# Kernel optimization log

Hardware: AMD Instinct MI355X
Metric: run time of the kernel (lower is better)

Reference implementation:

```python
import jax, jax.numpy as jnp
import numpy as np

N_NODES = 50000
N_EDGES = 800000
D = 128
N_GRAPHS = 128
N_CLASSES = 10
BN_EPS = 1e-5


def setup_inputs() -> dict:
    key = jax.random.key(0)
    ks = jax.random.split(key, 8)
    x = jax.random.normal(ks[0], (N_NODES, D), dtype=jnp.float32)
    edge_index = jax.random.randint(ks[1], (2, N_EDGES), 0, N_NODES, dtype=jnp.int64)
    batch = jnp.sort(jax.random.randint(ks[2], (N_NODES,), 0, N_GRAPHS, dtype=jnp.int64))
    s = 1.0 / np.sqrt(D)
    W1a = jax.random.normal(ks[3], (D, D), dtype=jnp.float32) * s
    W1b = jax.random.normal(ks[4], (D, D), dtype=jnp.float32) * s
    W2a = jax.random.normal(ks[5], (D, D), dtype=jnp.float32) * s
    W2b = jax.random.normal(ks[6], (D, D), dtype=jnp.float32) * s
    Wo = jax.random.normal(ks[7], (D, N_CLASSES), dtype=jnp.float32) * s
    z = jnp.zeros((D,), jnp.float32)
    o = jnp.ones((D,), jnp.float32)
    return dict(x=x, edge_index=edge_index, batch=batch,
                W1a=W1a, b1a=z, W1b=W1b, b1b=z, g1=o, be1=z,
                W2a=W2a, b2a=z, W2b=W2b, b2b=z, g2=o, be2=z,
                Wo=Wo, bo=jnp.zeros((N_CLASSES,), jnp.float32))


def _gin_conv(x, edge_index, Wa, ba, Wb, bb):
    # message passing: gather source features, scatter-add to targets (eps=0)
    msgs = x[edge_index[0]]                                   # [E, D]
    agg = jax.ops.segment_sum(msgs, edge_index[1], num_segments=x.shape[0])
    h = agg + x                                               # (1+eps)*x + sum_j x_j
    h = jnp.maximum(h @ Wa + ba, 0.0)                         # Linear -> ReLU
    return h @ Wb + bb                                        # Linear


def _bn_relu(h, gamma, beta):
    # BatchNorm1d (training mode: batch stats, biased var) + ReLU
    mu = jnp.mean(h, axis=0)
    var = jnp.mean(jnp.square(h - mu), axis=0)
    hn = (h - mu) * jax.lax.rsqrt(var + BN_EPS) * gamma + beta
    return jnp.maximum(hn, 0.0)


def reference(x, edge_index, batch,
              W1a, b1a, W1b, b1b, g1, be1,
              W2a, b2a, W2b, b2b, g2, be2,
              Wo, bo):
    h = _gin_conv(x, edge_index, W1a, b1a, W1b, b1b)
    h = _bn_relu(h, g1, be1)
    h = _gin_conv(h, edge_index, W2a, b2a, W2b, b2b)
    h = _bn_relu(h, g2, be2)
    pooled = jax.ops.segment_sum(h, batch, num_segments=N_GRAPHS)  # global_add_pool
    return pooled @ Wo + bo
```

## Files before the change

kernel.cpp:

```cpp
#include <hip/hip_runtime.h>

typedef __attribute__((ext_vector_type(8))) short bf16x8;
typedef __attribute__((ext_vector_type(4))) float f32x4;
typedef __attribute__((ext_vector_type(2))) float f32x2;
typedef __attribute__((ext_vector_type(2))) unsigned u32x2;
typedef __attribute__((ext_vector_type(4))) unsigned u32x4;

#define N_NODES 50000
#define N_EDGES 800000
#define DIM 128
#define N_GRAPHS 128
#define N_CLASSES 10
#define BN_EPS 1e-5f
#define FBLK ((N_NODES + 63) / 64)
#define FGRID (FBLK / 2)
#define NPART (FBLK * 4)
#define RED_NB 64
#define RED_ROWS ((NPART + RED_NB - 1) / RED_NB)

#define NBUCK 196
#define FILL_NB 400
#define FILL_PER (N_EDGES / FILL_NB)
#define BMAX 6144

#define CVT_NB (N_NODES * 64 / 256)
#define PREPW_NB 256

static __device__ __forceinline__ unsigned short f2bf(float f) {
    unsigned u = __float_as_uint(f);
    u += 0x7FFF + ((u >> 16) & 1);
    return (unsigned short)(u >> 16);
}
static __device__ __forceinline__ float bf_lo(unsigned u) { return __uint_as_float(u << 16); }
static __device__ __forceinline__ float bf_hi(unsigned u) { return __uint_as_float(u & 0xffff0000u); }
static __device__ __forceinline__ unsigned packbf(float a, float b) {
    return (unsigned)f2bf(a) | ((unsigned)f2bf(b) << 16);
}

__global__ __launch_bounds__(256) void prep_all(const f32x2* __restrict__ x,
                                                unsigned* __restrict__ xb,
                                                const float* __restrict__ W0,
                                                const float* __restrict__ W1,
                                                const float* __restrict__ W2,
                                                const float* __restrict__ W3,
                                                unsigned short* __restrict__ wf,
                                                const int* __restrict__ batch,
                                                int* __restrict__ gs,
                                                const int* __restrict__ ei,
                                                int* __restrict__ gbcnt,
                                                int* __restrict__ boff,
                                                int* __restrict__ gcur,
                                                int* __restrict__ ctr_scan) {
    int b = blockIdx.x, tid = threadIdx.x;
    if (b < CVT_NB) {
        int t = b * 256 + tid;
        f32x2 v = x[t];
        xb[t] = packbf(v[0], v[1]);
    } else if (b < CVT_NB + PREPW_NB) {
        int t = (b - CVT_NB) * 256 + tid;
        int m = t >> 14, rem = t & 16383;
        int e = rem & 7, lane = (rem >> 3) & 63, fi = rem >> 9;
        int ks = fi & 3, n = fi >> 2;
        int col = n * 16 + (lane & 15);
        int k = ks * 32 + ((lane >> 4) << 3) + e;
        const float* W = (m == 0) ? W0 : (m == 1) ? W1 : (m == 2) ? W2 : W3;
        wf[t] = f2bf(W[k * DIM + col]);
    } else if (b < CVT_NB + PREPW_NB + FILL_NB) {
        __shared__ int cnt[NBUCK];
        __shared__ int done;
        if (tid < NBUCK) cnt[tid] = 0;
        __syncthreads();
        int e0 = (b - CVT_NB - PREPW_NB) * FILL_PER;
        for (int c = tid; c < FILL_PER; c += 256) {
            int dst = ei[N_EDGES + e0 + c];
            atomicAdd(&cnt[dst >> 8], 1);
        }
        __syncthreads();
        if (tid < NBUCK) atomicAdd(&gbcnt[tid], cnt[tid]);
        __threadfence();
        __syncthreads();
        if (tid == 0) done = atomicAdd(ctr_scan, 1);
        __syncthreads();
        if (done == FILL_NB - 1) {
            __threadfence();
            __shared__ int buf[256];
            int v = (tid < NBUCK) ? gbcnt[tid] : 0;
            buf[tid] = v;
            __syncthreads();
#pragma unroll
            for (int off = 1; off < 256; off <<= 1) {
                int u = (tid >= off) ? buf[tid - off] : 0;
                __syncthreads();
                buf[tid] += u;
                __syncthreads();
            }
            if (tid < NBUCK) { int ex = buf[tid] - v; boff[tid] = ex; gcur[tid] = ex; }
            if (tid == 0) boff[NBUCK] = N_EDGES;
        }
    } else {
        int g = tid;
        if (g > N_GRAPHS) return;
        int lo = 0, hi = N_NODES;
        while (lo < hi) {
            int mid = (lo + hi) >> 1;
            if (batch[mid] < g) lo = mid + 1; else hi = mid;
        }
        gs[g] = lo;
    }
}

__global__ __launch_bounds__(256) void bucket_fill(const int* __restrict__ ei,
                                                   int* __restrict__ gcur,
                                                   unsigned* __restrict__ gbuf) {
    __shared__ unsigned ent[FILL_PER];
    __shared__ unsigned srt[FILL_PER];
    __shared__ int cnt[256], c2[256], lofs[256], gbase[256];
    int tid = threadIdx.x;
    int e0 = blockIdx.x * FILL_PER;
    cnt[tid] = 0; c2[tid] = 0;
    __syncthreads();
    for (int i = tid; i < FILL_PER; i += 256) {
        int src = ei[e0 + i];
        int dst = ei[N_EDGES + e0 + i];
        ent[i] = (unsigned)src | ((unsigned)(dst & 255) << 16) | ((unsigned)(dst >> 8) << 24);
        atomicAdd(&cnt[dst >> 8], 1);
    }
    __syncthreads();
    int v = cnt[tid];
    lofs[tid] = v;
    __syncthreads();
#pragma unroll
    for (int off = 1; off < 256; off <<= 1) {
        int u = (tid >= off) ? lofs[tid - off] : 0;
        __syncthreads();
        lofs[tid] += u;
        __syncthreads();
    }
    int excl = lofs[tid] - v;
    lofs[tid] = excl;
    if (tid < NBUCK && v > 0) gbase[tid] = atomicAdd(&gcur[tid], v);
    __syncthreads();
    for (int i = tid; i < FILL_PER; i += 256) {
        unsigned w = ent[i];
        int b = w >> 24;
        int r = atomicAdd(&c2[b], 1);
        srt[lofs[b] + r] = w;
    }
    __syncthreads();
    for (int i = tid; i < FILL_PER; i += 256) {
        unsigned w = srt[i];
        int b = w >> 24;
        gbuf[gbase[b] + (i - lofs[b])] = w;
    }
}

__global__ __launch_bounds__(256) void csr_build(const unsigned* __restrict__ gbuf,
                                                 const int* __restrict__ boff,
                                                 unsigned short* __restrict__ csr16,
                                                 int* __restrict__ row_start) {
    __shared__ unsigned ent[BMAX];
    __shared__ unsigned short csl[BMAX];
    __shared__ int cnt[256], c2[256], offs[256];
    int b = blockIdx.x, t = threadIdx.x;
    int base = boff[b], n = boff[b + 1] - base;
    for (int i = t; i < n; i += 256) ent[i] = gbuf[base + i];
    cnt[t] = 0; c2[t] = 0;
    __syncthreads();
    for (int i = t; i < n; i += 256) atomicAdd(&cnt[(ent[i] >> 16) & 255], 1);
    __syncthreads();
    int v = cnt[t];
    offs[t] = v;
    __syncthreads();
#pragma unroll
    for (int off = 1; off < 256; off <<= 1) {
        int u = (t >= off) ? offs[t - off] : 0;
        __syncthreads();
        offs[t] += u;
        __syncthreads();
    }
    int excl = offs[t] - v;
    int node = b * 256 + t;
    if (node < N_NODES) row_start[node] = base + excl;
    if (b == NBUCK - 1 && t == 0) row_start[N_NODES] = N_EDGES;
    __syncthreads();
    offs[t] = excl;
    __syncthreads();
    for (int i = t; i < n; i += 256) {
        unsigned w = ent[i];
        int d = (w >> 16) & 255;
        int r = atomicAdd(&c2[d], 1);
        csl[offs[d] + r] = (unsigned short)(w & 0xffffu);
    }
    __syncthreads();
    for (int i = t; i < n; i += 256) csr16[base + i] = csl[i];
}

template <bool BN>
__global__ __launch_bounds__(256) void aggregate_bf(const u32x4* __restrict__ F4,
                                                    u32x4* __restrict__ out,
                                                    const int* __restrict__ row_start,
                                                    const unsigned short* __restrict__ csr16,
                                                    const float* __restrict__ scale,
                                                    const float* __restrict__ shift) {
    int wave = threadIdx.x >> 6, lane = threadIdx.x & 63;
    int v = blockIdx.x * 4 + wave;
    if (v >= N_NODES) return;
    int q = lane >> 4;
    int c8 = lane & 15;
    f32x4 scA, scB, shA, shB;
    if (BN) {
        scA = ((const f32x4*)scale)[c8 * 2];
        scB = ((const f32x4*)scale)[c8 * 2 + 1];
        shA = ((const f32x4*)shift)[c8 * 2];
        shB = ((const f32x4*)shift)[c8 * 2 + 1];
    }
    int e0 = row_start[v];
    int n = row_start[v + 1] - e0;
    int myidx = (lane < n) ? (int)csr16[e0 + lane] : 0;
    int n64 = (n < 64) ? n : 64;

    float a[8] = {0.f, 0.f, 0.f, 0.f, 0.f, 0.f, 0.f, 0.f};
    float bacc[8] = {0.f, 0.f, 0.f, 0.f, 0.f, 0.f, 0.f, 0.f};

#define UNPACK8(U, P)                                                         \
    P[0] = bf_lo(U[0]); P[1] = bf_hi(U[0]); P[2] = bf_lo(U[1]); P[3] = bf_hi(U[1]); \
    P[4] = bf_lo(U[2]); P[5] = bf_hi(U[2]); P[6] = bf_lo(U[3]); P[7] = bf_hi(U[3]);
#define BN8(P)                                                                \
    if (BN) {                                                                 \
        P[0] = fmaxf(P[0] * scA[0] + shA[0], 0.f);                            \
        P[1] = fmaxf(P[1] * scA[1] + shA[1], 0.f);                            \
        P[2] = fmaxf(P[2] * scA[2] + shA[2], 0.f);                            \
        P[3] = fmaxf(P[3] * scA[3] + shA[3], 0.f);                            \
        P[4] = fmaxf(P[4] * scB[0] + shB[0], 0.f);                            \
        P[5] = fmaxf(P[5] * scB[1] + shB[1], 0.f);                            \
        P[6] = fmaxf(P[6] * scB[2] + shB[2], 0.f);                            \
        P[7] = fmaxf(P[7] * scB[3] + shB[3], 0.f);                            \
    }

    if (q == 0) {
        u32x4 u = F4[(size_t)v * 16 + c8];
        float p[8];
        UNPACK8(u, p)
        BN8(p)
#pragma unroll
        for (int k = 0; k < 8; ++k) a[k] += p[k];
    }

    for (int base = 0; base < n64; base += 8) {
        int j0 = base + q, j1 = base + 4 + q;
        int s0 = __shfl(myidx, j0 & 63, 64);
        int s1 = __shfl(myidx, j1 & 63, 64);
        u32x4 ua = F4[(size_t)s0 * 16 + c8];
        u32x4 ub = F4[(size_t)s1 * 16 + c8];
        float p[8], r[8];
        UNPACK8(ua, p)
        UNPACK8(ub, r)
        BN8(p)
        BN8(r)
        if (j0 < n64) {
#pragma unroll
            for (int k = 0; k < 8; ++k) a[k] += p[k];
        }
        if (j1 < n64) {
#pragma unroll
            for (int k = 0; k < 8; ++k) bacc[k] += r[k];
        }
    }
    for (int j = 64 + q; j < n; j += 4) {
        int s = csr16[e0 + j];
        u32x4 ua = F4[(size_t)s * 16 + c8];
        float p[8];
        UNPACK8(ua, p)
        BN8(p)
#pragma unroll
        for (int k = 0; k < 8; ++k) a[k] += p[k];
    }
#pragma unroll
    for (int k = 0; k < 8; ++k) a[k] += bacc[k];
#pragma unroll
    for (int k = 0; k < 8; ++k) {
        a[k] += __shfl_xor(a[k], 16, 64);
        a[k] += __shfl_xor(a[k], 32, 64);
    }
    if (q == 0) {
        u32x4 w;
        w[0] = packbf(a[0], a[1]);
        w[1] = packbf(a[2], a[3]);
        w[2] = packbf(a[4], a[5]);
        w[3] = packbf(a[6], a[7]);
        out[(size_t)v * 16 + c8] = w;
    }
#undef UNPACK8
#undef BN8
}

__global__ __launch_bounds__(256, 3) void fused_layer(
        const unsigned short* __restrict__ A,
        const bf16x8* __restrict__ wfA_g,
        const bf16x8* __restrict__ wfB_g,
        const float* __restrict__ bias_a,
        const float* __restrict__ bias_b,
        unsigned short* __restrict__ out,
        float* __restrict__ psum,
        float* __restrict__ psq, int M) {
    __shared__ bf16x8 wfS[2048];
    __shared__ unsigned short mid[8192];

    int tid = threadIdx.x;
    int w = tid >> 6, lane = tid & 63;
    int cl = lane & 15, kq = lane >> 4;

    bf16x8 wa[8], wb[8];
#pragma unroll
    for (int i = 0; i < 8; ++i) wa[i] = wfA_g[i * 256 + tid];
#pragma unroll
    for (int i = 0; i < 8; ++i) wb[i] = wfB_g[i * 256 + tid];

    for (int t = 0; t < 2; ++t) {
        int tile = blockIdx.x + t * FGRID;
        int rblk = tile * 64;

#pragma unroll
        for (int i = 0; i < 8; ++i) wfS[i * 256 + tid] = wa[i];

        int arow = rblk + w * 16 + cl;
        if (arow >= M) arow = M - 1;
        bf16x8 af[4];
        const unsigned short* Ap = A + (size_t)arow * DIM + kq * 8;
#pragma unroll
        for (int ks = 0; ks < 4; ++ks) af[ks] = *(const bf16x8*)(Ap + ks * 32);

        __syncthreads();

        f32x4 acc[8];
#pragma unroll
        for (int n = 0; n < 8; ++n) acc[n] = f32x4{0.f, 0.f, 0.f, 0.f};
#pragma unroll
        for (int n = 0; n < 8; ++n)
#pragma unroll
            for (int ks = 0; ks < 4; ++ks)
                acc[n] = __builtin_amdgcn_mfma_f32_16x16x32_bf16(
                    af[ks], wfS[(n * 4 + ks) * 64 + lane], acc[n], 0, 0, 0);

#pragma unroll
        for (int n = 0; n < 8; ++n) {
            int col = n * 16 + cl;
            float b = bias_a[col];
#pragma unroll
            for (int r = 0; r < 4; ++r) {
                int rl = w * 16 + kq * 4 + r;
                float v = fmaxf(acc[n][r] + b, 0.f);
                mid[(rl * DIM + col) ^ ((rl & 7) << 3)] = f2bf(v);
            }
        }
        __syncthreads();

#pragma unroll
        for (int i = 0; i < 8; ++i) wfS[i * 256 + tid] = wb[i];

        bf16x8 af2[4];
        {
            int rl = w * 16 + cl;
            int sw = (cl & 7) << 3;
#pragma unroll
            for (int ks = 0; ks < 4; ++ks)
                af2[ks] = *(const bf16x8*)(mid + ((rl * DIM + kq * 8 + ks * 32) ^ sw));
        }
        __syncthreads();

        f32x4 acc2[8];
#pragma unroll
        for (int n = 0; n < 8; ++n) acc2[n] = f32x4{0.f, 0.f, 0.f, 0.f};
#pragma unroll
        for (int n = 0; n < 8; ++n)
#pragma unroll
            for (int ks = 0; ks < 4; ++ks)
                acc2[n] = __builtin_amdgcn_mfma_f32_16x16x32_bf16(
                    af2[ks], wfS[(n * 4 + ks) * 64 + lane], acc2[n], 0, 0, 0);

        int prow = tile * 4 + w;
#pragma unroll
        for (int n = 0; n < 8; ++n) {
            int col = n * 16 + cl;
            float b = bias_b[col];
            float s = 0.f, q = 0.f;
#pragma unroll
            for (int r = 0; r < 4; ++r) {
                int rl = w * 16 + kq * 4 + r;
                float v = acc2[n][r] + b;
                if (rblk + rl < M) { s += v; q += v * v; }
                mid[(rl * DIM + col) ^ ((rl & 7) << 3)] = f2bf(v);
            }
            s += __shfl_xor(s, 16, 64);
            s += __shfl_xor(s, 32, 64);
            q += __shfl_xor(q, 16, 64);
            q += __shfl_xor(q, 32, 64);
            if (kq == 0) {
                psum[(size_t)prow * DIM + col] = s;
                psq[(size_t)prow * DIM + col] = q;
            }
        }

        {
            int r4 = lane >> 4, c = lane & 15;
#pragma unroll
            for (int rb = 0; rb < 4; ++rb) {
                int rl = w * 16 + rb * 4 + r4;
                int grow = rblk + rl;
                bf16x8 v = *(const bf16x8*)(mid + ((rl * DIM + c * 8) ^ ((rl & 7) << 3)));
                if (grow < M) *(bf16x8*)(out + (size_t)grow * DIM + c * 8) = v;
            }
        }
        __syncthreads();
    }
}

__global__ __launch_bounds__(256) void stats_all(const float* __restrict__ psum,
                                                 const float* __restrict__ psq,
                                                 float* __restrict__ ps2,
                                                 const float* __restrict__ g,
                                                 const float* __restrict__ be,
                                                 float* __restrict__ scale,
                                                 float* __restrict__ shift,
                                                 int* __restrict__ ctr) {
    int b = blockIdx.x, t = threadIdx.x;
    int c = t & 127;
    const float* src = (t < 128) ? psum : psq;
    int r0 = b * RED_ROWS;
    int r1 = min(NPART, r0 + RED_ROWS);
    float acc = 0.f;
    for (int r = r0; r < r1; ++r) acc += src[(size_t)r * DIM + c];
    ps2[(size_t)b * 256 + t] = acc;
    __threadfence();
    __shared__ int done;
    __syncthreads();
    if (t == 0) done = atomicAdd(ctr, 1);
    __syncthreads();
    if (done == RED_NB - 1) {
        __threadfence();
        float a2 = 0.f;
#pragma unroll 4
        for (int r = 0; r < RED_NB; ++r) a2 += ps2[(size_t)r * 256 + t];
        __shared__ float sums[128], sqs[128];
        if (t < 128) sums[c] = a2; else sqs[c] = a2;
        __syncthreads();
        if (t < 128) {
            const float invN = 1.0f / (float)N_NODES;
            float mu = sums[c] * invN;
            float var = sqs[c] * invN - mu * mu;
            float rs = rsqrtf(var + BN_EPS) * g[c];
            scale[c] = rs;
            shift[c] = be[c] - mu * rs;
        }
    }
}

__global__ __launch_bounds__(256) void bn_pool_final(const unsigned short* __restrict__ h,
                                                     const float* __restrict__ scale,
                                                     const float* __restrict__ shift,
                                                     const int* __restrict__ gs,
                                                     const float* __restrict__ Wo,
                                                     const float* __restrict__ bo,
                                                     float* __restrict__ out) {
    int g = blockIdx.x;
    int t = threadIdx.x;
    int c4 = t & 31;
    int rs = t >> 5;
    int r0 = gs[g], r1 = gs[g + 1];
    f32x4 sc = ((const f32x4*)scale)[c4];
    f32x4 sh = ((const f32x4*)shift)[c4];
    f32x4 acc = f32x4{0.f, 0.f, 0.f, 0.f};
    for (int r = r0 + rs; r < r1; r += 8) {
        u32x2 u = *(const u32x2*)(h + (size_t)r * DIM + c4 * 4);
        float f0 = bf_lo(u[0]), f1 = bf_hi(u[0]), f2 = bf_lo(u[1]), f3 = bf_hi(u[1]);
        acc[0] += fmaxf(f0 * sc[0] + sh[0], 0.f);
        acc[1] += fmaxf(f1 * sc[1] + sh[1], 0.f);
        acc[2] += fmaxf(f2 * sc[2] + sh[2], 0.f);
        acc[3] += fmaxf(f3 * sc[3] + sh[3], 0.f);
    }
    __shared__ f32x4 red[256];
    __shared__ float pf[DIM];
    red[t] = acc;
    __syncthreads();
#pragma unroll
    for (int off = 128; off >= 32; off >>= 1) {
        if (t < off) red[t] += red[t + off];
        __syncthreads();
    }
    if (t < 32) {
        f32x4 r = red[t];
        pf[t * 4 + 0] = r[0]; pf[t * 4 + 1] = r[1];
        pf[t * 4 + 2] = r[2]; pf[t * 4 + 3] = r[3];
    }
    __syncthreads();
    if (t < N_CLASSES) {
        float s = bo[t];
#pragma unroll 8
        for (int k = 0; k < DIM; ++k) s += pf[k] * Wo[k * N_CLASSES + t];
        out[g * N_CLASSES + t] = s;
    }
}

extern "C" void kernel_launch(void* const* d_in, const int* in_sizes, int n_in,
                              void* d_out, int out_size, void* d_ws, size_t ws_size,
                              hipStream_t stream) {
    const float* x   = (const float*)d_in[0];
    const int* ei    = (const int*)d_in[1];
    const int* batch = (const int*)d_in[2];
    const float* W1a = (const float*)d_in[3];
    const float* b1a = (const float*)d_in[4];
    const float* W1b = (const float*)d_in[5];
    const float* b1b = (const float*)d_in[6];
    const float* g1  = (const float*)d_in[7];
    const float* be1 = (const float*)d_in[8];
    const float* W2a = (const float*)d_in[9];
    const float* b2a = (const float*)d_in[10];
    const float* W2b = (const float*)d_in[11];
    const float* b2b = (const float*)d_in[12];
    const float* g2  = (const float*)d_in[13];
    const float* be2 = (const float*)d_in[14];
    const float* Wo  = (const float*)d_in[15];
    const float* bo  = (const float*)d_in[16];

    char* ws = (char*)d_ws;
    const size_t NBH = (size_t)N_NODES * DIM * 2;
    unsigned short* xb   = (unsigned short*)ws;
    unsigned short* aggb = (unsigned short*)(ws + NBH);
    unsigned short* hb   = (unsigned short*)(ws + 2 * NBH);
    unsigned short* wfrag = (unsigned short*)(ws + 3 * NBH);
    float* psum = (float*)(ws + 3 * NBH + 4 * 16384 * 2);
    float* psq  = psum + (size_t)NPART * DIM;
    float* ps2  = psq + (size_t)NPART * DIM;
    float* scale1  = ps2 + RED_NB * 256;
    float* shift1  = scale1 + 128;
    float* scale2  = scale1 + 256;
    float* shift2  = scale1 + 384;
    int* gs        = (int*)(shift2 + 128);
    int* gbcnt     = gs + N_GRAPHS + 1;
    int* ctrs      = gbcnt + NBUCK;
    int* boff      = ctrs + 3;
    int* gcur      = boff + NBUCK + 1;
    int* row_start = gcur + NBUCK;
    unsigned* gbuf = (unsigned*)(row_start + N_NODES + 1);
    unsigned short* csr16 = (unsigned short*)(gbuf + N_EDGES);

    hipMemsetAsync(gbcnt, 0, (NBUCK + 3) * 4, stream);

    prep_all<<<CVT_NB + PREPW_NB + FILL_NB + 1, 256, 0, stream>>>(
        (const f32x2*)x, (unsigned*)xb, W1a, W1b, W2a, W2b, wfrag, batch, gs, ei,
        gbcnt, boff, gcur, ctrs + 0);

    bucket_fill<<<FILL_NB, 256, 0, stream>>>(ei, gcur, gbuf);
    csr_build<<<NBUCK, 256, 0, stream>>>(gbuf, boff, csr16, row_start);

    const int ablk = (N_NODES + 3) / 4;

    aggregate_bf<false><<<ablk, 256, 0, stream>>>((const u32x4*)xb, (u32x4*)aggb,
                                                  row_start, csr16, nullptr, nullptr);
    fused_layer<<<FGRID, 256, 0, stream>>>(
        aggb, (const bf16x8*)(wfrag + 0 * 16384), (const bf16x8*)(wfrag + 1 * 16384),
        b1a, b1b, hb, psum, psq, N_NODES);
    stats_all<<<RED_NB, 256, 0, stream>>>(psum, psq, ps2, g1, be1, scale1, shift1,
                                          ctrs + 1);

    aggregate_bf<true><<<ablk, 256, 0, stream>>>((const u32x4*)hb, (u32x4*)aggb,
                                                 row_start, csr16, scale1, shift1);
    fused_layer<<<FGRID, 256, 0, stream>>>(
        aggb, (const bf16x8*)(wfrag + 2 * 16384), (const bf16x8*)(wfrag + 3 * 16384),
        b2a, b2b, hb, psum, psq, N_NODES);
    stats_all<<<RED_NB, 256, 0, stream>>>(psum, psq, ps2, g2, be2, scale2, shift2,
                                          ctrs + 2);

    bn_pool_final<<<N_GRAPHS, 256, 0, stream>>>(hb, scale2, shift2, gs, Wo, bo,
                                                (float*)d_out);
}
```

Measured before the change: 242.2 us.

## Replace last-block atomic reductions with separate kernels; unroll gather loop deeper

Removes the last-block-done pattern (a global atomic counter plus threadfences) from the bucket-count prefix scan and the BN stats reduction, and moves each finalize step into its own single-block kernel launch. This drops the counter memset and the per-block fence and atomic. The price is three extra kernel launches per forward. Separately, the neighbor-gather loop in the aggregation kernel now issues four row loads per iteration instead of two, putting more memory loads in flight per wave.

```diff
diff --git a/kernel.cpp b/kernel.cpp
--- a/kernel.cpp
+++ b/kernel.cpp
@@ -47,10 +47,7 @@
                                                 const int* __restrict__ batch,
                                                 int* __restrict__ gs,
                                                 const int* __restrict__ ei,
-                                                int* __restrict__ gbcnt,
-                                                int* __restrict__ boff,
-                                                int* __restrict__ gcur,
-                                                int* __restrict__ ctr_scan) {
+                                                int* __restrict__ gbcnt) {
     int b = blockIdx.x, tid = threadIdx.x;
     if (b < CVT_NB) {
         int t = b * 256 + tid;
@@ -67,7 +64,6 @@
         wf[t] = f2bf(W[k * DIM + col]);
     } else if (b < CVT_NB + PREPW_NB + FILL_NB) {
         __shared__ int cnt[NBUCK];
-        __shared__ int done;
         if (tid < NBUCK) cnt[tid] = 0;
         __syncthreads();
         int e0 = (b - CVT_NB - PREPW_NB) * FILL_PER;
@@ -77,26 +73,6 @@
         }
         __syncthreads();
         if (tid < NBUCK) atomicAdd(&gbcnt[tid], cnt[tid]);
-        __threadfence();
-        __syncthreads();
-        if (tid == 0) done = atomicAdd(ctr_scan, 1);
-        __syncthreads();
-        if (done == FILL_NB - 1) {
-            __threadfence();
-            __shared__ int buf[256];
-            int v = (tid < NBUCK) ? gbcnt[tid] : 0;
-            buf[tid] = v;
-            __syncthreads();
-#pragma unroll
-            for (int off = 1; off < 256; off <<= 1) {
-                int u = (tid >= off) ? buf[tid - off] : 0;
-                __syncthreads();
-                buf[tid] += u;
-                __syncthreads();
-            }
-            if (tid < NBUCK) { int ex = buf[tid] - v; boff[tid] = ex; gcur[tid] = ex; }
-            if (tid == 0) boff[NBUCK] = N_EDGES;
-        }
     } else {
         int g = tid;
         if (g > N_GRAPHS) return;
@@ -107,6 +83,25 @@
         }
         gs[g] = lo;
     }
+}
+
+__global__ __launch_bounds__(256) void bucket_scan(const int* __restrict__ gbcnt,
+                                                   int* __restrict__ boff,
+                                                   int* __restrict__ gcur) {
+    __shared__ int buf[256];
+    int t = threadIdx.x;
+    int v = (t < NBUCK) ? gbcnt[t] : 0;
+    buf[t] = v;
+    __syncthreads();
+#pragma unroll
+    for (int off = 1; off < 256; off <<= 1) {
+        int u = (t >= off) ? buf[t - off] : 0;
+        __syncthreads();
+        buf[t] += u;
+        __syncthreads();
+    }
+    if (t < NBUCK) { int ex = buf[t] - v; boff[t] = ex; gcur[t] = ex; }
+    if (t == 0) boff[NBUCK] = N_EDGES;
 }
 
 __global__ __launch_bounds__(256) void bucket_fill(const int* __restrict__ ei,
@@ -220,7 +215,7 @@
     int n64 = (n < 64) ? n : 64;
 
     float a[8] = {0.f, 0.f, 0.f, 0.f, 0.f, 0.f, 0.f, 0.f};
-    float bacc[8] = {0.f, 0.f, 0.f, 0.f, 0.f, 0.f, 0.f, 0.f};
+    float b2[8] = {0.f, 0.f, 0.f, 0.f, 0.f, 0.f, 0.f, 0.f};
 
 #define UNPACK8(U, P)                                                         \
     P[0] = bf_lo(U[0]); P[1] = bf_hi(U[0]); P[2] = bf_lo(U[1]); P[3] = bf_hi(U[1]); \
@@ -246,24 +241,40 @@
         for (int k = 0; k < 8; ++k) a[k] += p[k];
     }
 
-    for (int base = 0; base < n64; base += 8) {
-        int j0 = base + q, j1 = base + 4 + q;
+    for (int base = 0; base < n64; base += 16) {
+        int j0 = base + q, j1 = base + 4 + q, j2 = base + 8 + q, j3 = base + 12 + q;
         int s0 = __shfl(myidx, j0 & 63, 64);
         int s1 = __shfl(myidx, j1 & 63, 64);
+        int s2 = __shfl(myidx, j2 & 63, 64);
+        int s3 = __shfl(myidx, j3 & 63, 64);
         u32x4 ua = F4[(size_t)s0 * 16 + c8];
         u32x4 ub = F4[(size_t)s1 * 16 + c8];
-        float p[8], r[8];
-        UNPACK8(ua, p)
-        UNPACK8(ub, r)
-        BN8(p)
-        BN8(r)
+        u32x4 uc = F4[(size_t)s2 * 16 + c8];
+        u32x4 ud = F4[(size_t)s3 * 16 + c8];
+        float pa[8], pb[8], pc[8], pd[8];
+        UNPACK8(ua, pa)
+        UNPACK8(ub, pb)
+        UNPACK8(uc, pc)
+        UNPACK8(ud, pd)
+        BN8(pa)
+        BN8(pb)
+        BN8(pc)
+        BN8(pd)
         if (j0 < n64) {
 #pragma unroll
-            for (int k = 0; k < 8; ++k) a[k] += p[k];
+            for (int k = 0; k < 8; ++k) a[k] += pa[k];
         }
         if (j1 < n64) {
 #pragma unroll
-            for (int k = 0; k < 8; ++k) bacc[k] += r[k];
+            for (int k = 0; k < 8; ++k) b2[k] += pb[k];
+        }
+        if (j2 < n64) {
+#pragma unroll
+            for (int k = 0; k < 8; ++k) a[k] += pc[k];
+        }
+        if (j3 < n64) {
+#pragma unroll
+            for (int k = 0; k < 8; ++k) b2[k] += pd[k];
         }
     }
     for (int j = 64 + q; j < n; j += 4) {
@@ -276,7 +287,7 @@
         for (int k = 0; k < 8; ++k) a[k] += p[k];
     }
 #pragma unroll
-    for (int k = 0; k < 8; ++k) a[k] += bacc[k];
+    for (int k = 0; k < 8; ++k) a[k] += b2[k];
 #pragma unroll
     for (int k = 0; k < 8; ++k) {
         a[k] += __shfl_xor(a[k], 16, 64);
@@ -415,14 +426,9 @@
     }
 }
 
-__global__ __launch_bounds__(256) void stats_all(const float* __restrict__ psum,
-                                                 const float* __restrict__ psq,
-                                                 float* __restrict__ ps2,
-                                                 const float* __restrict__ g,
-                                                 const float* __restrict__ be,
-                                                 float* __restrict__ scale,
-                                                 float* __restrict__ shift,
-                                                 int* __restrict__ ctr) {
+__global__ __launch_bounds__(256) void reduce_stats(const float* __restrict__ psum,
+                                                    const float* __restrict__ psq,
+                                                    float* __restrict__ ps2) {
     int b = blockIdx.x, t = threadIdx.x;
     int c = t & 127;
     const float* src = (t < 128) ? psum : psq;
@@ -431,27 +437,28 @@
     float acc = 0.f;
     for (int r = r0; r < r1; ++r) acc += src[(size_t)r * DIM + c];
     ps2[(size_t)b * 256 + t] = acc;
-    __threadfence();
-    __shared__ int done;
-    __syncthreads();
-    if (t == 0) done = atomicAdd(ctr, 1);
-    __syncthreads();
-    if (done == RED_NB - 1) {
-        __threadfence();
-        float a2 = 0.f;
+}
+
+__global__ __launch_bounds__(256) void bn_finalize(const float* __restrict__ ps2,
+                                                   const float* __restrict__ g,
+                                                   const float* __restrict__ be,
+                                                   float* __restrict__ scale,
+                                                   float* __restrict__ shift) {
+    __shared__ float sums[128], sqs[128];
+    int t = threadIdx.x;
+    int c = t & 127;
+    float acc = 0.f;
 #pragma unroll 4
-        for (int r = 0; r < RED_NB; ++r) a2 += ps2[(size_t)r * 256 + t];
-        __shared__ float sums[128], sqs[128];
-        if (t < 128) sums[c] = a2; else sqs[c] = a2;
-        __syncthreads();
-        if (t < 128) {
-            const float invN = 1.0f / (float)N_NODES;
-            float mu = sums[c] * invN;
-            float var = sqs[c] * invN - mu * mu;
-            float rs = rsqrtf(var + BN_EPS) * g[c];
-            scale[c] = rs;
-            shift[c] = be[c] - mu * rs;
-        }
+    for (int r = 0; r < RED_NB; ++r) acc += ps2[(size_t)r * 256 + t];
+    if (t < 128) sums[c] = acc; else sqs[c] = acc;
+    __syncthreads();
+    if (t < 128) {
+        const float invN = 1.0f / (float)N_NODES;
+        float mu = sums[c] * invN;
+        float var = sqs[c] * invN - mu * mu;
+        float rs = rsqrtf(var + BN_EPS) * g[c];
+        scale[c] = rs;
+        shift[c] = be[c] - mu * rs;
     }
 }
 
@@ -537,19 +544,18 @@
     float* shift2  = scale1 + 384;
     int* gs        = (int*)(shift2 + 128);
     int* gbcnt     = gs + N_GRAPHS + 1;
-    int* ctrs      = gbcnt + NBUCK;
-    int* boff      = ctrs + 3;
+    int* boff      = gbcnt + NBUCK;
     int* gcur      = boff + NBUCK + 1;
     int* row_start = gcur + NBUCK;
     unsigned* gbuf = (unsigned*)(row_start + N_NODES + 1);
     unsigned short* csr16 = (unsigned short*)(gbuf + N_EDGES);
 
-    hipMemsetAsync(gbcnt, 0, (NBUCK + 3) * 4, stream);
+    hipMemsetAsync(gbcnt, 0, NBUCK * 4, stream);
 
     prep_all<<<CVT_NB + PREPW_NB + FILL_NB + 1, 256, 0, stream>>>(
-        (const f32x2*)x, (unsigned*)xb, W1a, W1b, W2a, W2b, wfrag, batch, gs, ei,
-        gbcnt, boff, gcur, ctrs + 0);
-
+        (const f32x2*)x, (unsigned*)xb, W1a, W1b, W2a, W2b, wfrag, batch, gs, ei, gbcnt);
+
+    bucket_scan<<<1, 256, 0, stream>>>(gbcnt, boff, gcur);
     bucket_fill<<<FILL_NB, 256, 0, stream>>>(ei, gcur, gbuf);
     csr_build<<<NBUCK, 256, 0, stream>>>(gbuf, boff, csr16, row_start);
 
@@ -560,16 +566,16 @@
     fused_layer<<<FGRID, 256, 0, stream>>>(
         aggb, (const bf16x8*)(wfrag + 0 * 16384), (const bf16x8*)(wfrag + 1 * 16384),
         b1a, b1b, hb, psum, psq, N_NODES);
-    stats_all<<<RED_NB, 256, 0, stream>>>(psum, psq, ps2, g1, be1, scale1, shift1,
-                                          ctrs + 1);
+    reduce_stats<<<RED_NB, 256, 0, stream>>>(psum, psq, ps2);
+    bn_finalize<<<1, 256, 0, stream>>>(ps2, g1, be1, scale1, shift1);
 
     aggregate_bf<true><<<ablk, 256, 0, stream>>>((const u32x4*)hb, (u32x4*)aggb,
                                                  row_start, csr16, scale1, shift1);
     fused_layer<<<FGRID, 256, 0, stream>>>(
         aggb, (const bf16x8*)(wfrag + 2 * 16384), (const bf16x8*)(wfrag + 3 * 16384),
         b2a, b2b, hb, psum, psq, N_NODES);
-    stats_all<<<RED_NB, 256, 0, stream>>>(psum, psq, ps2, g2, be2, scale2, shift2,
-                                          ctrs + 2);
+    reduce_stats<<<RED_NB, 256, 0, stream>>>(psum, psq, ps2);
+    bn_finalize<<<1, 256, 0, stream>>>(ps2, g2, be2, scale2, shift2);
 
     bn_pool_final<<<N_GRAPHS, 256, 0, stream>>>(hb, scale2, shift2, gs, Wo, bo,
                                                 (float*)d_out);
```

New measurement: 227.0 us. 6.3% less time.
